# Performance work log

Hardware: AMD Instinct MI355X
Metric: run time of the kernel (lower is better)

The kernel has to match this reference:

```python
import jax, jax.numpy as jnp
import numpy as np
from jax import lax

EMBED = 64


def setup_inputs() -> dict:
    key = jax.random.key(0)
    ks = jax.random.split(key, 5)
    b, l, v, e, h = 256, 1024, 96, 64, 256
    x = jax.random.randint(ks[0], (b, l), 0, v, dtype=jnp.int64)
    hidden = jnp.zeros((b, h), dtype=jnp.float32)
    # xavier-uniform-like init (scale by fan sums)
    emb = jax.random.normal(ks[1], (v, e), dtype=jnp.float32) * 0.1
    W_ih = jax.random.normal(ks[2], (e + h, h), dtype=jnp.float32) * (1.0 / np.sqrt(e + h))
    b_ih = jnp.zeros((h,), dtype=jnp.float32)
    W_ho = jax.random.normal(ks[3], (h, v), dtype=jnp.float32) * (1.0 / np.sqrt(h))
    b_ho = jnp.zeros((v,), dtype=jnp.float32)
    return {"x": x, "hidden": hidden, "emb": emb, "W_ih": W_ih, "b_ih": b_ih,
            "W_ho": W_ho, "b_ho": b_ho}


def reference(x, hidden, emb, W_ih, b_ih, W_ho, b_ho):
    # x: [b, l] int indices; hidden: [b, h]
    x_embed = emb[x]                      # [b, l, e]
    Wx, Wh = W_ih[:EMBED], W_ih[EMBED:]   # split cat([x, h]) @ W_ih
    # precompute input projections for all timesteps (batched GEMM)
    xproj = jnp.einsum('ble,eh->blh', x_embed, Wx) + b_ih  # [b, l, h]

    def step(h_prev, xp_t):
        h_t = jnp.tanh(xp_t + h_prev @ Wh)  # [b, h]
        return h_t, h_t

    final_hidden, hs = lax.scan(step, hidden, xproj.transpose(1, 0, 2))  # hs: [l, b, h]
    hs = hs.transpose(1, 0, 2)                     # [b, l, h]
    logits = jnp.einsum('blh,hv->blv', hs, W_ho) + b_ho  # [b, l, v]
    return logits, final_hidden
```

## Files before the change

kernel.cpp:

```cpp
#include <hip/hip_runtime.h>
#include <hip/hip_bf16.h>

#define Lv 1024
#define Vv 96
#define Ev 64
#define Hv 256
#define ROWS 16
#define HOFF (256 * 1024 * 96)
#define EPAD 72
#define HBUF (ROWS * Hv)

typedef __attribute__((ext_vector_type(8))) short bf16x8;
typedef __attribute__((ext_vector_type(4))) float f32x4;

__device__ __forceinline__ unsigned short f2b(float f) {
  unsigned u = __builtin_bit_cast(unsigned, f);
  return (unsigned short)((u + 0x7fffu + ((u >> 16) & 1u)) >> 16);
}
__device__ __forceinline__ unsigned cvtpk_bf16(float lo, float hi) {
  unsigned r;
  asm("v_cvt_pk_bf16_f32 %0, %1, %2" : "=v"(r) : "v"(lo), "v"(hi));
  return r;
}
__device__ __forceinline__ float fast_tanh(float x) {
  float e = __builtin_amdgcn_exp2f(x * 2.885390081777927f);
  return 1.0f - 2.0f * __builtin_amdgcn_rcpf(e + 1.0f);
}
__device__ __forceinline__ void step_barrier() {
  asm volatile("s_waitcnt lgkmcnt(0)\n\ts_barrier" ::: "memory");
  __builtin_amdgcn_sched_barrier(0);
}

__global__ void detect_i64(const int* __restrict__ x, int* __restrict__ flag) {
  if (threadIdx.x == 0 && blockIdx.x == 0) {
    int ok = 1;
    for (int i = 0; i < 64; ++i) ok &= (x[2 * i + 1] == 0);
    *flag = ok;
  }
}

__global__ __launch_bounds__(512, 2) void rnn_fused(
    const int* __restrict__ x, const float* __restrict__ h0,
    const float* __restrict__ emb, const float* __restrict__ W_ih,
    const float* __restrict__ b_ih, const float* __restrict__ W_ho,
    const float* __restrict__ b_ho, float* __restrict__ out,
    const int* __restrict__ flagp) {
  const int tid = threadIdx.x;
  const int w = tid >> 6, ln = tid & 63, lm = ln & 15, g = ln >> 4;
  const int r0 = blockIdx.x * ROWS;

  __shared__ __attribute__((aligned(16))) unsigned short s_emb[Vv * EPAD];
  __shared__ __attribute__((aligned(16))) unsigned short s_h[2 * HBUF];
  __shared__ unsigned char s_x[Lv * ROWS];

  const int flag = *flagp;

  for (int idx = tid; idx < Vv * Ev; idx += 512)
    s_emb[(idx >> 6) * EPAD + (idx & 63)] = f2b(emb[idx]);
  for (int idx = tid; idx < ROWS * Hv; idx += 512) {
    int m = idx >> 8, n = idx & 255;
    s_h[HBUF + (m << 8) + ((((n >> 3) ^ (m & 7)) << 3) | (n & 7))] =
        f2b(h0[(r0 + m) * Hv + n]);
  }
  for (int idx = tid; idx < ROWS * Lv; idx += 512) {
    int row = idx >> 10, t = idx & 1023;
    int src = (r0 + row) * Lv + t;
    int v = flag ? x[2 * src] : x[src];
    s_x[t * ROWS + row] = (unsigned char)v;
  }

  bf16x8 wh[2][8], wx[2][2], who[8];
  float bih[2], bhov = 0.0f;
#pragma unroll
  for (int nt = 0; nt < 2; ++nt) {
    const int n = 32 * w + 16 * nt + lm;
    bih[nt] = b_ih[n];
#pragma unroll
    for (int kf = 0; kf < 8; ++kf)
#pragma unroll
      for (int i = 0; i < 8; ++i)
        wh[nt][kf][i] = (short)f2b(W_ih[(Ev + 32 * kf + 8 * g + i) * Hv + n]);
#pragma unroll
    for (int kf = 0; kf < 2; ++kf)
#pragma unroll
      for (int i = 0; i < 8; ++i)
        wx[nt][kf][i] = (short)f2b(W_ih[(32 * kf + 8 * g + i) * Hv + n]);
  }
  if (w < 6) {
    const int n = 16 * w + lm;
    bhov = b_ho[n];
#pragma unroll
    for (int kf = 0; kf < 8; ++kf)
#pragma unroll
      for (int i = 0; i < 8; ++i)
        who[kf][i] = (short)f2b(W_ho[(32 * kf + 8 * g + i) * Vv + n]);
  }

  const unsigned short* ra[8];
#pragma unroll
  for (int kf = 0; kf < 8; ++kf)
    ra[kf] = &s_h[(lm << 8) + (((4 * kf + g) ^ (lm & 7)) << 3)];
  unsigned short* wa[8];
#pragma unroll
  for (int nt = 0; nt < 2; ++nt)
#pragma unroll
    for (int rr = 0; rr < 4; ++rr) {
      int m = 4 * g + rr, n = 32 * w + 16 * nt + lm;
      wa[nt * 4 + rr] = &s_h[(m << 8) + ((((n >> 3) ^ (m & 7)) << 3) | (n & 7))];
    }
  float* ob[4] = {out, out, out, out};
  if (w < 6) {
#pragma unroll
    for (int rr = 0; rr < 4; ++rr)
      ob[rr] = out + (size_t)(r0 + 4 * g + rr) * (Lv * Vv) + 16 * w + lm;
  }

  __syncthreads();

  bf16x8 ef0, ef1;
  {
    int xi = s_x[lm];
    const unsigned short* ep = &s_emb[xi * EPAD + 8 * g];
    ef0 = *(const bf16x8*)ep;
    ef1 = *(const bf16x8*)(ep + 32);
  }

#define STEP(TT, RB, WB, DOLOG, LAST)                                              \
  do {                                                                             \
    bf16x8 af[8];                                                                  \
    _Pragma("unroll") for (int kf = 0; kf < 8; ++kf)                               \
        af[kf] = *(const bf16x8*)(ra[kf] + (RB));                                  \
    f32x4 a0 = {bih[0], bih[0], bih[0], bih[0]};                                   \
    f32x4 a1 = {bih[1], bih[1], bih[1], bih[1]};                                   \
    a0 = __builtin_amdgcn_mfma_f32_16x16x32_bf16(ef0, wx[0][0], a0, 0, 0, 0);      \
    a1 = __builtin_amdgcn_mfma_f32_16x16x32_bf16(ef0, wx[1][0], a1, 0, 0, 0);      \
    a0 = __builtin_amdgcn_mfma_f32_16x16x32_bf16(ef1, wx[0][1], a0, 0, 0, 0);      \
    a1 = __builtin_amdgcn_mfma_f32_16x16x32_bf16(ef1, wx[1][1], a1, 0, 0, 0);      \
    _Pragma("unroll") for (int kf = 0; kf < 8; ++kf) {                             \
      a0 = __builtin_amdgcn_mfma_f32_16x16x32_bf16(af[kf], wh[0][kf], a0, 0, 0, 0);\
      a1 = __builtin_amdgcn_mfma_f32_16x16x32_bf16(af[kf], wh[1][kf], a1, 0, 0, 0);\
    }                                                                              \
    if ((DOLOG) && w < 6) {                                                        \
      f32x4 l = {bhov, bhov, bhov, bhov};                                          \
      _Pragma("unroll") for (int kf = 0; kf < 8; ++kf)                             \
          l = __builtin_amdgcn_mfma_f32_16x16x32_bf16(af[kf], who[kf], l, 0, 0, 0);\
      const size_t o = (size_t)((TT)-1) * Vv;                                      \
      ob[0][o] = l[0]; ob[1][o] = l[1]; ob[2][o] = l[2]; ob[3][o] = l[3];          \
    }                                                                              \
    {                                                                              \
      int tn = ((TT) + 1 < Lv) ? (TT) + 1 : (Lv - 1);                              \
      int xi = s_x[tn * ROWS + lm];                                                \
      const unsigned short* ep = &s_emb[xi * EPAD + 8 * g];                        \
      ef0 = *(const bf16x8*)ep;                                                    \
      ef1 = *(const bf16x8*)(ep + 32);                                             \
    }                                                                              \
    float th0 = fast_tanh(a0[0]), th1 = fast_tanh(a0[1]);                          \
    float th2 = fast_tanh(a0[2]), th3 = fast_tanh(a0[3]);                          \
    float th4 = fast_tanh(a1[0]), th5 = fast_tanh(a1[1]);                          \
    float th6 = fast_tanh(a1[2]), th7 = fast_tanh(a1[3]);                          \
    unsigned p01 = cvtpk_bf16(th0, th1), p23 = cvtpk_bf16(th2, th3);               \
    unsigned p45 = cvtpk_bf16(th4, th5), p67 = cvtpk_bf16(th6, th7);               \
    wa[0][WB] = (unsigned short)p01;                                               \
    wa[1][WB] = (unsigned short)(p01 >> 16);                                       \
    wa[2][WB] = (unsigned short)p23;                                               \
    wa[3][WB] = (unsigned short)(p23 >> 16);                                       \
    wa[4][WB] = (unsigned short)p45;                                               \
    wa[5][WB] = (unsigned short)(p45 >> 16);                                       \
    wa[6][WB] = (unsigned short)p67;                                               \
    wa[7][WB] = (unsigned short)(p67 >> 16);                                       \
    if (LAST) {                                                                    \
      float* fh = out + HOFF + (size_t)(r0 + 4 * g) * Hv + 32 * w + lm;            \
      fh[0 * Hv] = th0; fh[1 * Hv] = th1; fh[2 * Hv] = th2; fh[3 * Hv] = th3;      \
      fh[0 * Hv + 16] = th4; fh[1 * Hv + 16] = th5;                                \
      fh[2 * Hv + 16] = th6; fh[3 * Hv + 16] = th7;                                \
    }                                                                              \
    step_barrier();                                                                \
  } while (0)

  STEP(0, HBUF, 0, 0, 0);
  for (int t = 1; t < Lv - 1; t += 2) {
    STEP(t, 0, HBUF, 1, 0);
    STEP(t + 1, HBUF, 0, 1, 0);
  }
  STEP(Lv - 1, 0, HBUF, 1, 1);

  if (w < 6) {
    bf16x8 af[8];
#pragma unroll
    for (int kf = 0; kf < 8; ++kf) af[kf] = *(const bf16x8*)(ra[kf] + HBUF);
    f32x4 l = {bhov, bhov, bhov, bhov};
#pragma unroll
    for (int kf = 0; kf < 8; ++kf)
      l = __builtin_amdgcn_mfma_f32_16x16x32_bf16(af[kf], who[kf], l, 0, 0, 0);
    const size_t o = (size_t)(Lv - 1) * Vv;
    ob[0][o] = l[0]; ob[1][o] = l[1]; ob[2][o] = l[2]; ob[3][o] = l[3];
  }
#undef STEP
}

extern "C" void kernel_launch(void* const* d_in, const int* in_sizes, int n_in,
                              void* d_out, int out_size, void* d_ws, size_t ws_size,
                              hipStream_t stream) {
  const int* x     = (const int*)d_in[0];
  const float* h0  = (const float*)d_in[1];
  const float* emb = (const float*)d_in[2];
  const float* Wih = (const float*)d_in[3];
  const float* bih = (const float*)d_in[4];
  const float* Who = (const float*)d_in[5];
  const float* bho = (const float*)d_in[6];
  float* out = (float*)d_out;
  int* flag = (int*)d_ws;

  detect_i64<<<1, 64, 0, stream>>>(x, flag);
  rnn_fused<<<16, 512, 0, stream>>>(x, h0, emb, Wih, bih, Who, bho, out, flag);
}
```

Measured before the change: 751.0 us.

## Halve waves per block, transpose MFMA operands, stream embeddings from global memory

```diff
diff --git a/kernel.cpp b/kernel.cpp
--- a/kernel.cpp
+++ b/kernel.cpp
@@ -7,11 +7,12 @@
 #define Hv 256
 #define ROWS 16
 #define HOFF (256 * 1024 * 96)
-#define EPAD 72
-#define HBUF (ROWS * Hv)
+#define HBUF 4096
 
 typedef __attribute__((ext_vector_type(8))) short bf16x8;
 typedef __attribute__((ext_vector_type(4))) float f32x4;
+typedef __attribute__((ext_vector_type(2))) unsigned int u32x2;
+typedef __attribute__((ext_vector_type(4))) unsigned int u32x4;
 
 __device__ __forceinline__ unsigned short f2b(float f) {
   unsigned u = __builtin_bit_cast(unsigned, f);
@@ -21,6 +22,14 @@
   unsigned r;
   asm("v_cvt_pk_bf16_f32 %0, %1, %2" : "=v"(r) : "v"(lo), "v"(hi));
   return r;
+}
+__device__ __forceinline__ bf16x8 pack8(f32x4 a, f32x4 b) {
+  u32x4 t;
+  t[0] = cvtpk_bf16(a[0], a[1]);
+  t[1] = cvtpk_bf16(a[2], a[3]);
+  t[2] = cvtpk_bf16(b[0], b[1]);
+  t[3] = cvtpk_bf16(b[2], b[3]);
+  return __builtin_bit_cast(bf16x8, t);
 }
 __device__ __forceinline__ float fast_tanh(float x) {
   float e = __builtin_amdgcn_exp2f(x * 2.885390081777927f);
@@ -39,7 +48,7 @@
   }
 }
 
-__global__ __launch_bounds__(512, 2) void rnn_fused(
+__global__ __launch_bounds__(256, 1) void rnn_fused(
     const int* __restrict__ x, const float* __restrict__ h0,
     const float* __restrict__ emb, const float* __restrict__ W_ih,
     const float* __restrict__ b_ih, const float* __restrict__ W_ho,
@@ -49,32 +58,19 @@
   const int w = tid >> 6, ln = tid & 63, lm = ln & 15, g = ln >> 4;
   const int r0 = blockIdx.x * ROWS;
 
-  __shared__ __attribute__((aligned(16))) unsigned short s_emb[Vv * EPAD];
   __shared__ __attribute__((aligned(16))) unsigned short s_h[2 * HBUF];
-  __shared__ unsigned char s_x[Lv * ROWS];
-
-  const int flag = *flagp;
-
-  for (int idx = tid; idx < Vv * Ev; idx += 512)
-    s_emb[(idx >> 6) * EPAD + (idx & 63)] = f2b(emb[idx]);
-  for (int idx = tid; idx < ROWS * Hv; idx += 512) {
-    int m = idx >> 8, n = idx & 255;
-    s_h[HBUF + (m << 8) + ((((n >> 3) ^ (m & 7)) << 3) | (n & 7))] =
-        f2b(h0[(r0 + m) * Hv + n]);
-  }
-  for (int idx = tid; idx < ROWS * Lv; idx += 512) {
-    int row = idx >> 10, t = idx & 1023;
-    int src = (r0 + row) * Lv + t;
-    int v = flag ? x[2 * src] : x[src];
-    s_x[t * ROWS + row] = (unsigned char)v;
-  }
-
-  bf16x8 wh[2][8], wx[2][2], who[8];
-  float bih[2], bhov = 0.0f;
-#pragma unroll
-  for (int nt = 0; nt < 2; ++nt) {
-    const int n = 32 * w + 16 * nt + lm;
-    bih[nt] = b_ih[n];
+
+  for (int idx = tid; idx < ROWS * Hv; idx += 256) {
+    int b_ = idx >> 8, hd = idx & 255;
+    s_h[HBUF + b_ * 256 + ((((hd >> 3) ^ (b_ & 7)) << 3) | (hd & 7))] =
+        f2b(h0[(r0 + b_) * Hv + hd]);
+  }
+
+  bf16x8 wh[4][8], wx[4][2], who[2][8];
+  f32x4 bihv[4], bhv[2];
+#pragma unroll
+  for (int nt = 0; nt < 4; ++nt) {
+    const int n = 64 * w + 16 * nt + lm;
 #pragma unroll
     for (int kf = 0; kf < 8; ++kf)
 #pragma unroll
@@ -85,96 +81,113 @@
 #pragma unroll
       for (int i = 0; i < 8; ++i)
         wx[nt][kf][i] = (short)f2b(W_ih[(32 * kf + 8 * g + i) * Hv + n]);
-  }
-  if (w < 6) {
-    const int n = 16 * w + lm;
-    bhov = b_ho[n];
-#pragma unroll
-    for (int kf = 0; kf < 8; ++kf)
-#pragma unroll
-      for (int i = 0; i < 8; ++i)
-        who[kf][i] = (short)f2b(W_ho[(32 * kf + 8 * g + i) * Vv + n]);
-  }
+    bihv[nt] = *(const f32x4*)&b_ih[64 * w + 16 * nt + 4 * g];
+  }
+  const int njt = (w < 2) ? 2 : 1;
+  const int jtb = (w < 2) ? 2 * w : (w + 2);
+#pragma unroll
+  for (int j = 0; j < 2; ++j)
+    if (j < njt) {
+      const int nv = 16 * (jtb + j) + lm;
+#pragma unroll
+      for (int kf = 0; kf < 8; ++kf)
+#pragma unroll
+        for (int i = 0; i < 8; ++i)
+          who[j][kf][i] = (short)f2b(W_ho[(32 * kf + 8 * g + i) * Vv + nv]);
+      bhv[j] = *(const f32x4*)&b_ho[16 * (jtb + j) + 4 * g];
+    }
 
   const unsigned short* ra[8];
 #pragma unroll
   for (int kf = 0; kf < 8; ++kf)
-    ra[kf] = &s_h[(lm << 8) + (((4 * kf + g) ^ (lm & 7)) << 3)];
-  unsigned short* wa[8];
-#pragma unroll
-  for (int nt = 0; nt < 2; ++nt)
-#pragma unroll
-    for (int rr = 0; rr < 4; ++rr) {
-      int m = 4 * g + rr, n = 32 * w + 16 * nt + lm;
-      wa[nt * 4 + rr] = &s_h[(m << 8) + ((((n >> 3) ^ (m & 7)) << 3) | (n & 7))];
-    }
-  float* ob[4] = {out, out, out, out};
-  if (w < 6) {
-#pragma unroll
-    for (int rr = 0; rr < 4; ++rr)
-      ob[rr] = out + (size_t)(r0 + 4 * g + rr) * (Lv * Vv) + 16 * w + lm;
-  }
+    ra[kf] = &s_h[lm * 256 + (((4 * kf + g) ^ (lm & 7)) << 3)];
+  unsigned short* wa[4];
+#pragma unroll
+  for (int nt = 0; nt < 4; ++nt)
+    wa[nt] = &s_h[lm * 256 + (((8 * w + 2 * nt + (g >> 1)) ^ (lm & 7)) << 3) +
+                  ((g & 1) << 2)];
+  float* lptr[2] = {out, out};
+#pragma unroll
+  for (int j = 0; j < 2; ++j)
+    if (j < njt)
+      lptr[j] = out + (size_t)(r0 + lm) * (Lv * Vv) + 16 * (jtb + j) + 4 * g;
+
+  const int flag = *flagp;
+  const long long xoff = (long long)(r0 + lm) * Lv;
+  const int* xp = x + (flag ? 2 * xoff : xoff);
+  const int xstr = flag ? 2 : 1;
 
   __syncthreads();
 
-  bf16x8 ef0, ef1;
+  f32x4 pe0, pe1, pe2, pe3;
+  int xi_n;
   {
-    int xi = s_x[lm];
-    const unsigned short* ep = &s_emb[xi * EPAD + 8 * g];
-    ef0 = *(const bf16x8*)ep;
-    ef1 = *(const bf16x8*)(ep + 32);
-  }
-
-#define STEP(TT, RB, WB, DOLOG, LAST)                                              \
-  do {                                                                             \
-    bf16x8 af[8];                                                                  \
-    _Pragma("unroll") for (int kf = 0; kf < 8; ++kf)                               \
-        af[kf] = *(const bf16x8*)(ra[kf] + (RB));                                  \
-    f32x4 a0 = {bih[0], bih[0], bih[0], bih[0]};                                   \
-    f32x4 a1 = {bih[1], bih[1], bih[1], bih[1]};                                   \
-    a0 = __builtin_amdgcn_mfma_f32_16x16x32_bf16(ef0, wx[0][0], a0, 0, 0, 0);      \
-    a1 = __builtin_amdgcn_mfma_f32_16x16x32_bf16(ef0, wx[1][0], a1, 0, 0, 0);      \
-    a0 = __builtin_amdgcn_mfma_f32_16x16x32_bf16(ef1, wx[0][1], a0, 0, 0, 0);      \
-    a1 = __builtin_amdgcn_mfma_f32_16x16x32_bf16(ef1, wx[1][1], a1, 0, 0, 0);      \
-    _Pragma("unroll") for (int kf = 0; kf < 8; ++kf) {                             \
-      a0 = __builtin_amdgcn_mfma_f32_16x16x32_bf16(af[kf], wh[0][kf], a0, 0, 0, 0);\
-      a1 = __builtin_amdgcn_mfma_f32_16x16x32_bf16(af[kf], wh[1][kf], a1, 0, 0, 0);\
-    }                                                                              \
-    if ((DOLOG) && w < 6) {                                                        \
-      f32x4 l = {bhov, bhov, bhov, bhov};                                          \
-      _Pragma("unroll") for (int kf = 0; kf < 8; ++kf)                             \
-          l = __builtin_amdgcn_mfma_f32_16x16x32_bf16(af[kf], who[kf], l, 0, 0, 0);\
-      const size_t o = (size_t)((TT)-1) * Vv;                                      \
-      ob[0][o] = l[0]; ob[1][o] = l[1]; ob[2][o] = l[2]; ob[3][o] = l[3];          \
-    }                                                                              \
-    {                                                                              \
-      int tn = ((TT) + 1 < Lv) ? (TT) + 1 : (Lv - 1);                              \
-      int xi = s_x[tn * ROWS + lm];                                                \
-      const unsigned short* ep = &s_emb[xi * EPAD + 8 * g];                        \
-      ef0 = *(const bf16x8*)ep;                                                    \
-      ef1 = *(const bf16x8*)(ep + 32);                                             \
-    }                                                                              \
-    float th0 = fast_tanh(a0[0]), th1 = fast_tanh(a0[1]);                          \
-    float th2 = fast_tanh(a0[2]), th3 = fast_tanh(a0[3]);                          \
-    float th4 = fast_tanh(a1[0]), th5 = fast_tanh(a1[1]);                          \
-    float th6 = fast_tanh(a1[2]), th7 = fast_tanh(a1[3]);                          \
-    unsigned p01 = cvtpk_bf16(th0, th1), p23 = cvtpk_bf16(th2, th3);               \
-    unsigned p45 = cvtpk_bf16(th4, th5), p67 = cvtpk_bf16(th6, th7);               \
-    wa[0][WB] = (unsigned short)p01;                                               \
-    wa[1][WB] = (unsigned short)(p01 >> 16);                                       \
-    wa[2][WB] = (unsigned short)p23;                                               \
-    wa[3][WB] = (unsigned short)(p23 >> 16);                                       \
-    wa[4][WB] = (unsigned short)p45;                                               \
-    wa[5][WB] = (unsigned short)(p45 >> 16);                                       \
-    wa[6][WB] = (unsigned short)p67;                                               \
-    wa[7][WB] = (unsigned short)(p67 >> 16);                                       \
-    if (LAST) {                                                                    \
-      float* fh = out + HOFF + (size_t)(r0 + 4 * g) * Hv + 32 * w + lm;            \
-      fh[0 * Hv] = th0; fh[1 * Hv] = th1; fh[2 * Hv] = th2; fh[3 * Hv] = th3;      \
-      fh[0 * Hv + 16] = th4; fh[1 * Hv + 16] = th5;                                \
-      fh[2 * Hv + 16] = th6; fh[3 * Hv + 16] = th7;                                \
-    }                                                                              \
-    step_barrier();                                                                \
+    int xi0 = xp[0];
+    xi_n = xp[xstr];
+    const float* ep = &emb[xi0 * Ev + 8 * g];
+    pe0 = *(const f32x4*)ep;
+    pe1 = *(const f32x4*)(ep + 4);
+    pe2 = *(const f32x4*)(ep + 32);
+    pe3 = *(const f32x4*)(ep + 36);
+  }
+
+#define STEP(TT, RB, WB, DOLOG, LAST)                                             \
+  do {                                                                            \
+    bf16x8 ef0 = pack8(pe0, pe1), ef1 = pack8(pe2, pe3);                          \
+    bf16x8 af[8];                                                                 \
+    _Pragma("unroll") for (int kf = 0; kf < 8; ++kf)                              \
+        af[kf] = *(const bf16x8*)(ra[kf] + (RB));                                 \
+    f32x4 aA[4], aB[4];                                                           \
+    _Pragma("unroll") for (int nt = 0; nt < 4; ++nt) {                            \
+      aA[nt] = bihv[nt];                                                          \
+      aB[nt] = (f32x4){0.f, 0.f, 0.f, 0.f};                                       \
+    }                                                                             \
+    _Pragma("unroll") for (int kf = 0; kf < 4; ++kf)                              \
+        _Pragma("unroll") for (int nt = 0; nt < 4; ++nt)                          \
+        aA[nt] = __builtin_amdgcn_mfma_f32_16x16x32_bf16(wh[nt][kf], af[kf],      \
+                                                         aA[nt], 0, 0, 0);        \
+    _Pragma("unroll") for (int kf = 4; kf < 8; ++kf)                              \
+        _Pragma("unroll") for (int nt = 0; nt < 4; ++nt)                          \
+        aB[nt] = __builtin_amdgcn_mfma_f32_16x16x32_bf16(wh[nt][kf], af[kf],      \
+                                                         aB[nt], 0, 0, 0);        \
+    if (DOLOG) {                                                                  \
+      _Pragma("unroll") for (int j = 0; j < 2; ++j) if (j < njt) {                \
+        f32x4 l = bhv[j];                                                         \
+        _Pragma("unroll") for (int kf = 0; kf < 8; ++kf)                          \
+            l = __builtin_amdgcn_mfma_f32_16x16x32_bf16(who[j][kf], af[kf], l,    \
+                                                        0, 0, 0);                 \
+        *(f32x4*)lptr[j] = l;                                                     \
+        lptr[j] += Vv;                                                            \
+      }                                                                           \
+    }                                                                             \
+    {                                      \
+      const float* ep = &emb[xi_n * Ev + 8 * g];                                  \
+      pe0 = *(const f32x4*)ep;                                                    \
+      pe1 = *(const f32x4*)(ep + 4);                                              \
+      pe2 = *(const f32x4*)(ep + 32);                                             \
+      pe3 = *(const f32x4*)(ep + 36);                                             \
+      int tn = ((TT) + 2 < Lv) ? (TT) + 2 : (Lv - 1);                             \
+      xi_n = xp[tn * xstr];                                                       \
+    }                                                                             \
+    _Pragma("unroll") for (int nt = 0; nt < 4; ++nt)                              \
+        aA[nt] = __builtin_amdgcn_mfma_f32_16x16x32_bf16(wx[nt][0], ef0, aA[nt],  \
+                                                         0, 0, 0);                \
+    _Pragma("unroll") for (int nt = 0; nt < 4; ++nt)                              \
+        aB[nt] = __builtin_amdgcn_mfma_f32_16x16x32_bf16(wx[nt][1], ef1, aB[nt],  \
+                                                         0, 0, 0);                \
+    _Pragma("unroll") for (int nt = 0; nt < 4; ++nt) {                            \
+      f32x4 hv;                                                                   \
+      _Pragma("unroll") for (int rr = 0; rr < 4; ++rr)                            \
+          hv[rr] = fast_tanh(aA[nt][rr] + aB[nt][rr]);                            \
+      u32x2 p;                                                                    \
+      p[0] = cvtpk_bf16(hv[0], hv[1]);                                            \
+      p[1] = cvtpk_bf16(hv[2], hv[3]);                                            \
+      *(u32x2*)(wa[nt] + (WB)) = p;                                               \
+      if (LAST)                                                                   \
+        *(f32x4*)(out + HOFF + (size_t)(r0 + lm) * Hv + 64 * w + 16 * nt +        \
+                  4 * g) = hv;                                                    \
+    }                                                                             \
+    step_barrier();                                                               \
   } while (0)
 
   STEP(0, HBUF, 0, 0, 0);
@@ -184,16 +197,20 @@
   }
   STEP(Lv - 1, 0, HBUF, 1, 1);
 
-  if (w < 6) {
+  {
     bf16x8 af[8];
 #pragma unroll
     for (int kf = 0; kf < 8; ++kf) af[kf] = *(const bf16x8*)(ra[kf] + HBUF);
-    f32x4 l = {bhov, bhov, bhov, bhov};
-#pragma unroll
-    for (int kf = 0; kf < 8; ++kf)
-      l = __builtin_amdgcn_mfma_f32_16x16x32_bf16(af[kf], who[kf], l, 0, 0, 0);
-    const size_t o = (size_t)(Lv - 1) * Vv;
-    ob[0][o] = l[0]; ob[1][o] = l[1]; ob[2][o] = l[2]; ob[3][o] = l[3];
+#pragma unroll
+    for (int j = 0; j < 2; ++j)
+      if (j < njt) {
+        f32x4 l = bhv[j];
+#pragma unroll
+        for (int kf = 0; kf < 8; ++kf)
+          l = __builtin_amdgcn_mfma_f32_16x16x32_bf16(who[j][kf], af[kf], l, 0,
+                                                      0, 0);
+        *(f32x4*)lptr[j] = l;
+      }
   }
 #undef STEP
 }
@@ -212,5 +229,5 @@
   int* flag = (int*)d_ws;
 
   detect_i64<<<1, 64, 0, stream>>>(x, flag);
-  rnn_fused<<<16, 512, 0, stream>>>(x, h0, emb, Wih, bih, Who, bho, out, flag);
-}
+  rnn_fused<<<16, 256, 0, stream>>>(x, h0, emb, Wih, bih, Who, bho, out, flag);
+}
```

Measured after the change: 1.098 ms. 46.3% more time.

## Split RNN recurrence from output projection and widen recurrence blocks to 1024 threads

Applied to the files above, without the earlier changes.

```diff
diff --git a/kernel.cpp b/kernel.cpp
--- a/kernel.cpp
+++ b/kernel.cpp
@@ -8,10 +8,11 @@
 #define ROWS 16
 #define HOFF (256 * 1024 * 96)
 #define EPAD 72
-#define HBUF (ROWS * Hv)
+#define HB 4096
 
 typedef __attribute__((ext_vector_type(8))) short bf16x8;
 typedef __attribute__((ext_vector_type(4))) float f32x4;
+typedef __attribute__((ext_vector_type(2))) unsigned int u32x2;
 
 __device__ __forceinline__ unsigned short f2b(float f) {
   unsigned u = __builtin_bit_cast(unsigned, f);
@@ -39,7 +40,179 @@
   }
 }
 
-__global__ __launch_bounds__(512, 2) void rnn_fused(
+__global__ __launch_bounds__(1024, 1) void rnn16(
+    const int* __restrict__ x, const float* __restrict__ h0,
+    const float* __restrict__ emb, const float* __restrict__ W_ih,
+    const float* __restrict__ b_ih, float* __restrict__ out,
+    unsigned short* __restrict__ hs, const int* __restrict__ flagp) {
+  const int tid = threadIdx.x;
+  const int w = tid >> 6, ln = tid & 63, lm = ln & 15, g = ln >> 4;
+  const int r0 = blockIdx.x * ROWS;
+
+  __shared__ __attribute__((aligned(16))) unsigned short s_h[2 * HB];
+  __shared__ __attribute__((aligned(16))) unsigned short s_emb[Vv * EPAD];
+  __shared__ unsigned char s_x[Lv * ROWS];
+
+  const int flag = *flagp;
+
+  for (int idx = tid; idx < Vv * Ev; idx += 1024)
+    s_emb[(idx >> 6) * EPAD + (idx & 63)] = f2b(emb[idx]);
+  for (int idx = tid; idx < ROWS * Hv; idx += 1024) {
+    int b_ = idx >> 8, hd = idx & 255;
+    s_h[HB + b_ * 256 + ((((hd >> 3) ^ (b_ & 7)) << 3) | (hd & 7))] =
+        f2b(h0[(r0 + b_) * Hv + hd]);
+  }
+  for (int idx = tid; idx < ROWS * Lv; idx += 1024) {
+    int t = idx >> 4, row = idx & 15;
+    long long src = (long long)(r0 + row) * Lv + t;
+    int v = flag ? x[2 * src] : x[src];
+    s_x[t * ROWS + row] = (unsigned char)v;
+  }
+
+  bf16x8 wh[8], wx[2];
+  const int n = 16 * w + lm;
+#pragma unroll
+  for (int kf = 0; kf < 8; ++kf)
+#pragma unroll
+    for (int i = 0; i < 8; ++i)
+      wh[kf][i] = (short)f2b(W_ih[(Ev + 32 * kf + 8 * g + i) * Hv + n]);
+#pragma unroll
+  for (int kf = 0; kf < 2; ++kf)
+#pragma unroll
+    for (int i = 0; i < 8; ++i)
+      wx[kf][i] = (short)f2b(W_ih[(32 * kf + 8 * g + i) * Hv + n]);
+  const float bih = b_ih[n];
+
+  const unsigned short* ra[8];
+#pragma unroll
+  for (int kf = 0; kf < 8; ++kf)
+    ra[kf] = &s_h[lm * 256 + (((4 * kf + g) ^ (lm & 7)) << 3)];
+  unsigned short* wa[4];
+#pragma unroll
+  for (int rr = 0; rr < 4; ++rr) {
+    int b_ = 4 * g + rr;
+    wa[rr] = &s_h[b_ * 256 + ((((2 * w + (lm >> 3)) ^ (b_ & 7)) << 3) | (lm & 7))];
+  }
+  const unsigned short* ea =
+      &s_h[w * 256 + ((((ln >> 1) ^ (w & 7)) << 3) | ((ln & 1) << 2))];
+  unsigned short* hp = hs + (size_t)(r0 + w) * 256 + ln * 4;
+
+  __syncthreads();
+
+  bf16x8 ef0, ef1;
+  int xi_n;
+  {
+    int xi0 = s_x[lm];
+    const unsigned short* ep = &s_emb[xi0 * EPAD + 8 * g];
+    ef0 = *(const bf16x8*)ep;
+    ef1 = *(const bf16x8*)(ep + 32);
+    xi_n = s_x[ROWS + lm];
+  }
+
+#define STEP(TT, RBe, WBe, EXPORT, LAST)                                          \
+  do {                                                                            \
+    if (EXPORT) {                      \
+      u32x2 ev = *(const u32x2*)(ea + (RBe));                                     \
+      *(u32x2*)hp = ev;                                                           \
+      hp += (size_t)Hv * 256;                                                     \
+    }                                                                             \
+    bf16x8 af[8];                                                                 \
+    _Pragma("unroll") for (int kf = 0; kf < 8; ++kf)                              \
+        af[kf] = *(const bf16x8*)(ra[kf] + (RBe));                                \
+    f32x4 aA = {bih, bih, bih, bih};                                              \
+    f32x4 aB = {0.f, 0.f, 0.f, 0.f};                                              \
+    aA = __builtin_amdgcn_mfma_f32_16x16x32_bf16(ef0, wx[0], aA, 0, 0, 0);        \
+    aB = __builtin_amdgcn_mfma_f32_16x16x32_bf16(ef1, wx[1], aB, 0, 0, 0);        \
+    _Pragma("unroll") for (int kf = 0; kf < 4; ++kf)                              \
+        aA = __builtin_amdgcn_mfma_f32_16x16x32_bf16(af[kf], wh[kf], aA, 0, 0, 0);\
+    _Pragma("unroll") for (int kf = 4; kf < 8; ++kf)                              \
+        aB = __builtin_amdgcn_mfma_f32_16x16x32_bf16(af[kf], wh[kf], aB, 0, 0, 0);\
+    {                                      \
+      const unsigned short* ep = &s_emb[xi_n * EPAD + 8 * g];                     \
+      ef0 = *(const bf16x8*)ep;                                                   \
+      ef1 = *(const bf16x8*)(ep + 32);                                            \
+      int tn = ((TT) + 2 < Lv) ? (TT) + 2 : (Lv - 1);                             \
+      xi_n = s_x[tn * ROWS + lm];                                                 \
+    }                                                                             \
+    float hv0 = fast_tanh(aA[0] + aB[0]), hv1 = fast_tanh(aA[1] + aB[1]);         \
+    float hv2 = fast_tanh(aA[2] + aB[2]), hv3 = fast_tanh(aA[3] + aB[3]);         \
+    unsigned p01 = cvtpk_bf16(hv0, hv1), p23 = cvtpk_bf16(hv2, hv3);              \
+    wa[0][WBe] = (unsigned short)p01;                                             \
+    wa[1][WBe] = (unsigned short)(p01 >> 16);                                     \
+    wa[2][WBe] = (unsigned short)p23;                                             \
+    wa[3][WBe] = (unsigned short)(p23 >> 16);                                     \
+    if (LAST) {                                                                   \
+      float* fo = out + HOFF + (size_t)(r0 + 4 * g) * Hv + n;                     \
+      fo[0 * Hv] = hv0; fo[1 * Hv] = hv1; fo[2 * Hv] = hv2; fo[3 * Hv] = hv3;     \
+    }                                                                             \
+    step_barrier();                                                               \
+  } while (0)
+
+  STEP(0, HB, 0, 0, 0);
+  for (int t = 1; t < Lv - 1; t += 2) {
+    STEP(t, 0, HB, 1, 0);
+    STEP(t + 1, HB, 0, 1, 0);
+  }
+  STEP(Lv - 1, 0, HB, 1, 1);
+
+  {
+    u32x2 ev = *(const u32x2*)(ea + HB);
+    *(u32x2*)hp = ev;
+  }
+#undef STEP
+}
+
+__global__ __launch_bounds__(512, 2) void logits_gemm(
+    const unsigned short* __restrict__ hs, const float* __restrict__ W_ho,
+    const float* __restrict__ b_ho, float* __restrict__ out) {
+  const int tid = threadIdx.x;
+  const int w = tid >> 6, ln = tid & 63, lm = ln & 15, g = ln >> 4;
+  const int tg = blockIdx.x >> 2, bg = blockIdx.x & 3;
+
+  __shared__ __attribute__((aligned(16))) unsigned short s_who[3072 * 8];
+  for (int f = tid; f < 3072; f += 512) {
+    int vt = f >> 9, kf = (f >> 6) & 7, lane = f & 63;
+    int k0 = 32 * kf + 8 * (lane >> 4), v = 16 * vt + (lane & 15);
+    bf16x8 fr;
+#pragma unroll
+    for (int i = 0; i < 8; ++i) fr[i] = (short)f2b(W_ho[(k0 + i) * Vv + v]);
+    *(bf16x8*)&s_who[f * 8] = fr;
+  }
+  __syncthreads();
+
+  const int bt = w & 3, vg = w >> 2;
+  const int b0 = bg * 64 + bt * 16;
+  const int j0 = vg * 3;
+  float bb[3];
+#pragma unroll
+  for (int jj = 0; jj < 3; ++jj) bb[jj] = b_ho[16 * (j0 + jj) + lm];
+
+#pragma unroll
+  for (int tt = 0; tt < 4; ++tt) {
+    const int t = tg * 4 + tt;
+    const unsigned short* hpb = hs + (size_t)t * (256 * 256) + (b0 + lm) * 256 + 8 * g;
+    f32x4 acc[3];
+#pragma unroll
+    for (int jj = 0; jj < 3; ++jj) acc[jj] = (f32x4){bb[jj], bb[jj], bb[jj], bb[jj]};
+#pragma unroll
+    for (int kf = 0; kf < 8; ++kf) {
+      bf16x8 af = *(const bf16x8*)(hpb + 32 * kf);
+#pragma unroll
+      for (int jj = 0; jj < 3; ++jj) {
+        bf16x8 bw = *(const bf16x8*)&s_who[(((j0 + jj) * 8 + kf) * 64 + ln) * 8];
+        acc[jj] = __builtin_amdgcn_mfma_f32_16x16x32_bf16(af, bw, acc[jj], 0, 0, 0);
+      }
+    }
+#pragma unroll
+    for (int jj = 0; jj < 3; ++jj)
+#pragma unroll
+      for (int rr = 0; rr < 4; ++rr)
+        out[(size_t)(b0 + 4 * g + rr) * (Lv * Vv) + (size_t)t * Vv +
+            16 * (j0 + jj) + lm] = acc[jj][rr];
+  }
+}
+
+__global__ __launch_bounds__(512, 2) void rnn8(
     const int* __restrict__ x, const float* __restrict__ h0,
     const float* __restrict__ emb, const float* __restrict__ W_ih,
     const float* __restrict__ b_ih, const float* __restrict__ W_ho,
@@ -50,7 +223,7 @@
   const int r0 = blockIdx.x * ROWS;
 
   __shared__ __attribute__((aligned(16))) unsigned short s_emb[Vv * EPAD];
-  __shared__ __attribute__((aligned(16))) unsigned short s_h[2 * HBUF];
+  __shared__ __attribute__((aligned(16))) unsigned short s_h[2 * HB];
   __shared__ unsigned char s_x[Lv * ROWS];
 
   const int flag = *flagp;
@@ -58,13 +231,13 @@
   for (int idx = tid; idx < Vv * Ev; idx += 512)
     s_emb[(idx >> 6) * EPAD + (idx & 63)] = f2b(emb[idx]);
   for (int idx = tid; idx < ROWS * Hv; idx += 512) {
-    int m = idx >> 8, n = idx & 255;
-    s_h[HBUF + (m << 8) + ((((n >> 3) ^ (m & 7)) << 3) | (n & 7))] =
-        f2b(h0[(r0 + m) * Hv + n]);
+    int m = idx >> 8, nn = idx & 255;
+    s_h[HB + (m << 8) + ((((nn >> 3) ^ (m & 7)) << 3) | (nn & 7))] =
+        f2b(h0[(r0 + m) * Hv + nn]);
   }
   for (int idx = tid; idx < ROWS * Lv; idx += 512) {
     int row = idx >> 10, t = idx & 1023;
-    int src = (r0 + row) * Lv + t;
+    long long src = (long long)(r0 + row) * Lv + t;
     int v = flag ? x[2 * src] : x[src];
     s_x[t * ROWS + row] = (unsigned char)v;
   }
@@ -125,7 +298,7 @@
     ef1 = *(const bf16x8*)(ep + 32);
   }
 
-#define STEP(TT, RB, WB, DOLOG, LAST)                                              \
+#define STEP8(TT, RB, WB, DOLOG, LAST)                                             \
   do {                                                                             \
     bf16x8 af[8];                                                                  \
     _Pragma("unroll") for (int kf = 0; kf < 8; ++kf)                               \
@@ -174,20 +347,21 @@
       fh[0 * Hv + 16] = th4; fh[1 * Hv + 16] = th5;                                \
       fh[2 * Hv + 16] = th6; fh[3 * Hv + 16] = th7;                                \
     }                                                                              \
-    step_barrier();                                                                \
+    asm volatile("s_waitcnt lgkmcnt(0)\n\ts_barrier" ::: "memory");                \
+    __builtin_amdgcn_sched_barrier(0);                                             \
   } while (0)
 
-  STEP(0, HBUF, 0, 0, 0);
+  STEP8(0, HB, 0, 0, 0);
   for (int t = 1; t < Lv - 1; t += 2) {
-    STEP(t, 0, HBUF, 1, 0);
-    STEP(t + 1, HBUF, 0, 1, 0);
-  }
-  STEP(Lv - 1, 0, HBUF, 1, 1);
+    STEP8(t, 0, HB, 1, 0);
+    STEP8(t + 1, HB, 0, 1, 0);
+  }
+  STEP8(Lv - 1, 0, HB, 1, 1);
 
   if (w < 6) {
     bf16x8 af[8];
 #pragma unroll
-    for (int kf = 0; kf < 8; ++kf) af[kf] = *(const bf16x8*)(ra[kf] + HBUF);
+    for (int kf = 0; kf < 8; ++kf) af[kf] = *(const bf16x8*)(ra[kf] + HB);
     f32x4 l = {bhov, bhov, bhov, bhov};
 #pragma unroll
     for (int kf = 0; kf < 8; ++kf)
@@ -195,7 +369,7 @@
     const size_t o = (size_t)(Lv - 1) * Vv;
     ob[0][o] = l[0]; ob[1][o] = l[1]; ob[2][o] = l[2]; ob[3][o] = l[3];
   }
-#undef STEP
+#undef STEP8
 }
 
 extern "C" void kernel_launch(void* const* d_in, const int* in_sizes, int n_in,
@@ -211,6 +385,13 @@
   float* out = (float*)d_out;
   int* flag = (int*)d_ws;
 
+  const size_t hs_bytes = (size_t)Lv * 256 * 256 * 2;
   detect_i64<<<1, 64, 0, stream>>>(x, flag);
-  rnn_fused<<<16, 512, 0, stream>>>(x, h0, emb, Wih, bih, Who, bho, out, flag);
-}
+  if (ws_size >= hs_bytes + 256) {
+    unsigned short* hsp = (unsigned short*)((char*)d_ws + 256);
+    rnn16<<<16, 1024, 0, stream>>>(x, h0, emb, Wih, bih, out, hsp, flag);
+    logits_gemm<<<1024, 512, 0, stream>>>(hsp, Who, bho, out);
+  } else {
+    rnn8<<<16, 512, 0, stream>>>(x, h0, emb, Wih, bih, Who, bho, out, flag);
+  }
+}
```

Result: slower. 891.4 us (+18.7%).
